# Performance work log

Measured on AMD Instinct MI355X. Metric: run time of the kernel, lower is better.

The kernel has to match this reference:

```python
import jax, jax.numpy as jnp
import numpy as np

KS = 5          # kernel_size per pseudo-dim
DIM = 2         # pseudo-coordinate dims
KTOT = KS ** DIM  # 25 spline kernel slots
N_NODES = 50000
N_EDGES = 1600000
N_GRAPHS = 64
F_IN, H1, H2, N_CLS = 32, 32, 64, 10


def spline_basis(edge_attr):
    """Open B-spline basis, degree 1, dim=2, kernel_size=5.
    Returns basis [E,4] and flat kernel indices [E,4]."""
    v = edge_attr * (KS - 1)                    # [E,2] in [0, KS-1]
    lo = jnp.floor(v)
    frac = v - lo                               # [E,2]
    lo_i = lo.astype(jnp.int32)
    # per-dim basis values for offsets s in {0,1}: (1-frac), frac
    bas_d = jnp.stack([1.0 - frac, frac], axis=-1)            # [E,2,2]
    idx_d = jnp.minimum(lo_i[..., None] + jnp.arange(2, dtype=jnp.int32), KS - 1)  # [E,2,2]
    basis = bas_d[:, 0, :, None] * bas_d[:, 1, None, :]       # [E,2,2]
    kidx = idx_d[:, 0, :, None] + KS * idx_d[:, 1, None, :]   # [E,2,2]
    E = edge_attr.shape[0]
    return basis.reshape(E, 4), kidx.reshape(E, 4)


def spline_conv(x, src, dst, basis, kidx, W, Wroot, b):
    """SplineConv: gather x[src], spline-weight, scatter-mean to dst, + root + bias.
    W: [KTOT, Cin, Cout]."""
    N, Cin = x.shape
    x_j = x[src]                                # [E, Cin] gather
    # accumulate per-(node, kernel-slot) weighted sums; loop over 4 nonzero combos
    T = jnp.zeros((N * KTOT, Cin), dtype=x.dtype)
    for s in range(4):
        seg = dst * KTOT + kidx[:, s]
        T = T + jax.ops.segment_sum(basis[:, s, None] * x_j, seg,
                                    num_segments=N * KTOT)
    T = T.reshape(N, KTOT, Cin)
    out = jnp.einsum('nki,kio->no', T, W)       # [N, Cout]
    deg = jax.ops.segment_sum(jnp.ones_like(dst, dtype=x.dtype), dst,
                              num_segments=N)
    out = out / jnp.maximum(deg, 1.0)[:, None]  # aggr='mean'
    return out + x @ Wroot + b


def global_mean_pool(x, batch, num_graphs):
    s = jax.ops.segment_sum(x, batch, num_segments=num_graphs)
    cnt = jax.ops.segment_sum(jnp.ones((x.shape[0],), x.dtype), batch,
                              num_segments=num_graphs)
    return s / jnp.maximum(cnt, 1.0)[:, None]


def setup_inputs() -> dict:
    key = jax.random.key(0)
    ks = jax.random.split(key, 16)
    x = jax.random.normal(ks[0], (N_NODES, F_IN), jnp.float32)
    edge_index = jax.random.randint(ks[1], (2, N_EDGES), 0, N_NODES, jnp.int32)
    edge_attr = jax.random.uniform(ks[2], (N_EDGES, DIM), jnp.float32)
    batch = jnp.sort(jax.random.randint(ks[3], (N_NODES,), 0, N_GRAPHS, jnp.int32))

    def w(k, shape, fan_in):
        return jax.random.normal(k, shape, jnp.float32) / np.sqrt(fan_in)

    return {
        'x': x, 'edge_index': edge_index, 'edge_attr': edge_attr, 'batch': batch,
        'W1': w(ks[4], (KTOT, F_IN, H1), F_IN), 'root1': w(ks[5], (F_IN, H1), F_IN),
        'b1': jnp.zeros((H1,), jnp.float32),
        'W2': w(ks[6], (KTOT, H1, H2), H1), 'root2': w(ks[7], (H1, H2), H1),
        'b2': jnp.zeros((H2,), jnp.float32),
        'lin1_w': w(ks[8], (H2, 64), H2), 'lin1_b': jnp.zeros((64,), jnp.float32),
        'lin2_w': w(ks[9], (64, 64), 64), 'lin2_b': jnp.zeros((64,), jnp.float32),
        'lin3_w': w(ks[10], (64, N_CLS), 64), 'lin3_b': jnp.zeros((N_CLS,), jnp.float32),
    }


def reference(x, edge_index, edge_attr, batch, W1, root1, b1, W2, root2, b2,
              lin1_w, lin1_b, lin2_w, lin2_b, lin3_w, lin3_b):
    src, dst = edge_index[0], edge_index[1]
    basis, kidx = spline_basis(edge_attr)
    h = jax.nn.relu(spline_conv(x, src, dst, basis, kidx, W1, root1, b1))
    h = jax.nn.relu(spline_conv(h, src, dst, basis, kidx, W2, root2, b2))
    g = global_mean_pool(h, batch, N_GRAPHS)                # [B, 64]
    g = g * jax.nn.sigmoid(g @ lin1_w + lin1_b)
    g = g * jax.nn.sigmoid(g @ lin2_w + lin2_b)
    return jax.nn.log_softmax(g @ lin3_w + lin3_b, axis=1)  # [B, N_CLS]
```

## Files before the change

kernel.cpp:

```cpp
#include <hip/hip_runtime.h>
#include <hip/hip_bf16.h>
#include <hip/hip_fp16.h>
#include <cstdint>


typedef _Float16 half8 __attribute__((ext_vector_type(8)));
typedef float f32x4 __attribute__((ext_vector_type(4)));

__device__ __forceinline__ int h2_as_int(__half2 h) {
  int v; __builtin_memcpy(&v, &h, 4); return v;
}
__device__ __forceinline__ __half2 int_as_h2(int v) {
  __half2 h; __builtin_memcpy(&h, &v, 4); return h;
}

__device__ __forceinline__ int lowb(const int* __restrict__ a, int n, int v) {
  int lo = 0, hi = n;
  while (lo < hi) { int m = (lo + hi) >> 1; if (a[m] < v) lo = m + 1; else hi = m; }
  return lo;
}

__global__ void hist_kernel(const int* __restrict__ dst, int E, int* __restrict__ deg) {
  int e = blockIdx.x * 256 + threadIdx.x;
  if (e < E) atomicAdd(&deg[dst[e]], 1);
}

__global__ __launch_bounds__(1024) void scan_block_kernel(
    const int* __restrict__ deg, int n, int* __restrict__ offs, int* __restrict__ bsums) {
  __shared__ int wsum[16];
  int t = threadIdx.x;
  int gi = blockIdx.x * 1024 + t;
  int v = (gi < n) ? deg[gi] : 0;
  int lane = t & 63, w = t >> 6;
  int x = v;
  #pragma unroll
  for (int d = 1; d < 64; d <<= 1) { int y = __shfl_up(x, d, 64); if (lane >= d) x += y; }
  if (lane == 63) wsum[w] = x;
  __syncthreads();
  if (w == 0) {
    int s = (lane < 16) ? wsum[lane] : 0;
    #pragma unroll
    for (int d = 1; d < 16; d <<= 1) { int y = __shfl_up(s, d, 64); if (lane >= d) s += y; }
    if (lane < 16) wsum[lane] = s;
  }
  __syncthreads();
  int add = (w > 0) ? wsum[w - 1] : 0;
  x += add;
  if (gi < n) offs[gi + 1] = x;
  if (t == 1023) bsums[blockIdx.x] = x;
}

__global__ __launch_bounds__(64) void scan_bsums_kernel(
    const int* __restrict__ bsums, int nb, int* __restrict__ boff) {
  int l = threadIdx.x;
  int v = (l < nb) ? bsums[l] : 0;
  int x = v;
  #pragma unroll
  for (int d = 1; d < 64; d <<= 1) { int y = __shfl_up(x, d, 64); if (l >= d) x += y; }
  if (l < nb) boff[l] = x - v;
}

__global__ void scan_add_kernel(int* __restrict__ offs, const int* __restrict__ boff, int n) {
  int i = blockIdx.x * 256 + threadIdx.x;
  if (i < n) offs[i + 1] += boff[i >> 10];
  if (i == 0) offs[0] = 0;
}

__global__ void scatter_kernel(const int* __restrict__ src, const int* __restrict__ dst,
                               const float2* __restrict__ attr, int E,
                               const int* __restrict__ offs, int* __restrict__ cursor,
                               int4* __restrict__ emeta) {
  int e = blockIdx.x * 256 + threadIdx.x;
  if (e < E) {
    float2 a = attr[e];
    float v0 = a.x * 4.f, v1 = a.y * 4.f;
    int i00 = min((int)v0, 3);
    int i10 = min((int)v1, 3);
    float f0 = v0 - (float)i00;
    float f1 = v1 - (float)i10;
    float w00 = (1.f - f0) * (1.f - f1);
    float w10 = f0 * (1.f - f1);
    float w01 = (1.f - f0) * f1;
    float w11 = f0 * f1;
    int d = dst[e];
    int p = offs[d] + atomicAdd(&cursor[d], 1);
    emeta[p] = make_int4(src[e], (i10 * 5 + i00) | (i10 << 5),
                         h2_as_int(__floats2half2_rn(w00, w10)),
                         h2_as_int(__floats2half2_rn(w01, w11)));
  }
}

__global__ void x2h_kernel(const float* __restrict__ X, __half* __restrict__ Xh, int n) {
  int i = blockIdx.x * 256 + threadIdx.x;
  if (i < n) Xh[i] = __float2half(X[i]);
}

__global__ void w2h_kernel(const float* __restrict__ W, __half* __restrict__ Wh,
                           int ncolTot, int COUT) {
  int idx = blockIdx.x * 256 + threadIdx.x;
  if (idx < ncolTot * 32) {
    int col = idx >> 5, i = idx & 31;
    int kk = col / COUT, ch = col - kk * COUT;
    Wh[idx] = __float2half(W[(kk * 32 + i) * COUT + ch]);
  }
}

__global__ __launch_bounds__(256) void mfma_ygemm(
    const __half* __restrict__ Xh, const __half* __restrict__ Wh,
    __half* __restrict__ Y, int N, int ncol, int strideY) {
  __shared__ __half Ls[16 * 264];
  const int t = threadIdx.x;
  const int w = t >> 6, lane = t & 63;
  const int rowBase = blockIdx.x * 16;
  const int colBase = blockIdx.y * 256;
  const int kOff = (lane >> 4) * 8;
  int arow = min(rowBase + (lane & 15), N - 1);
  const half8 Af = *(const half8*)(Xh + (size_t)arow * 32 + kOff);
  half8 Bf[4];
  #pragma unroll
  for (int c = 0; c < 4; ++c) {
    int col = min(colBase + w * 64 + c * 16 + (lane & 15), ncol - 1);
    Bf[c] = *(const half8*)(Wh + (size_t)col * 32 + kOff);
  }
  f32x4 zero = {0.f, 0.f, 0.f, 0.f};
  f32x4 acc[4];
  #pragma unroll
  for (int c = 0; c < 4; ++c)
    acc[c] = __builtin_amdgcn_mfma_f32_16x16x32_f16(Af, Bf[c], zero, 0, 0, 0);
  #pragma unroll
  for (int c = 0; c < 4; ++c) {
    int col = w * 64 + c * 16 + (lane & 15);
    int r0 = (lane >> 4) * 4;
    #pragma unroll
    for (int r = 0; r < 4; ++r)
      Ls[(r0 + r) * 264 + col] = __float2half(acc[c][r]);
  }
  __syncthreads();
  int row = rowBase + (t >> 4);
  int cseg = (t & 15) * 16;
  if (row < N && colBase + cseg < ncol) {
    int4* dst = (int4*)(Y + (size_t)row * (size_t)strideY + colBase + cseg);
    const int4* srcp = (const int4*)(Ls + (t >> 4) * 264 + cseg);
    dst[0] = srcp[0];
    dst[1] = srcp[1];
  }
}

template <int COUT>
__global__ __launch_bounds__(256) void gather_kernel(
    const int4* __restrict__ emeta, const int* __restrict__ offs,
    const __half* __restrict__ Y, int strideY,
    float* __restrict__ hagg, int N, int g0, int g1, int first, int fused,
    const __half* __restrict__ X, const float* __restrict__ root,
    const float* __restrict__ bias, __half* __restrict__ hout) {
  __shared__ float Rs[32 * COUT];
  const int t = threadIdx.x;
  if (fused) {
    #pragma unroll
    for (int q = 0; q < (8 * COUT) / 256; ++q)
      *(float4*)&Rs[(t + q * 256) * 4] = *(const float4*)&root[(t + q * 256) * 4];
    __syncthreads();
  }
  const int w = t >> 6, lane = t & 63;
  const int n = blockIdx.x * 4 + w;
  if (n >= N) return;
  const int q4 = lane >> 4, r = lane & 15;
  const int di0 = q4 & 1, di1 = q4 >> 1;
  constexpr int CPL = COUT / 16;
  const int laneByte = (di1 * 5 * COUT + di0 * COUT + r * CPL) * 2;
  const char* Ybase = (const char*)Y;
  float acc[CPL];
  #pragma unroll
  for (int j = 0; j < CPL; ++j) acc[j] = 0.f;
  const int beg = offs[n], end = offs[n + 1];
  for (int b0 = beg; b0 < end; b0 += 64) {
    const int cnt = min(64, end - b0);
    int4 m = emeta[b0 + min(lane, cnt - 1)];
    const int i10 = m.y >> 5;
    const bool valid = (lane < cnt) & (i10 >= g0) & (i10 < g1);
    int myByte = (m.x * strideY + ((m.y & 31) - g0 * 5) * COUT) * 2;
    int myP0 = m.z, myP1 = m.w;
    unsigned long long mask = __ballot(valid);
    while (mask) {
      int j = (int)__builtin_ctzll(mask);
      mask &= mask - 1;
      int b  = __builtin_amdgcn_readlane(myByte, j);
      int p0 = __builtin_amdgcn_readlane(myP0, j);
      int p1 = __builtin_amdgcn_readlane(myP1, j);
      __half2 wp = int_as_h2(di1 ? p1 : p0);
      float wq = __half2float(di0 ? __high2half(wp) : __low2half(wp));
      const __half* yp = (const __half*)(Ybase + (size_t)(unsigned)(b + laneByte));
      if constexpr (CPL == 2) {
        __half2 yv = *(const __half2*)yp;
        acc[0] = fmaf(wq, __half2float(__low2half(yv)), acc[0]);
        acc[1] = fmaf(wq, __half2float(__high2half(yv)), acc[1]);
      } else {
        __half2 ya = *(const __half2*)yp;
        __half2 yb = *(const __half2*)(yp + 2);
        acc[0] = fmaf(wq, __half2float(__low2half(ya)), acc[0]);
        acc[1] = fmaf(wq, __half2float(__high2half(ya)), acc[1]);
        acc[2] = fmaf(wq, __half2float(__low2half(yb)), acc[2]);
        acc[3] = fmaf(wq, __half2float(__high2half(yb)), acc[3]);
      }
    }
  }
  #pragma unroll
  for (int j = 0; j < CPL; ++j) {
    acc[j] += __shfl_xor(acc[j], 16);
    acc[j] += __shfl_xor(acc[j], 32);
  }
  const int laneCh = r * CPL;
  if (lane < 16) {
    if (!fused) {
      float* hp = hagg + (size_t)n * COUT + laneCh;
      if constexpr (CPL == 2) {
        float2 o = make_float2(acc[0], acc[1]);
        if (!first) { float2 p = *(float2*)hp; o.x += p.x; o.y += p.y; }
        *(float2*)hp = o;
      } else {
        float4 o = make_float4(acc[0], acc[1], acc[2], acc[3]);
        if (!first) {
          float4 p = *(float4*)hp;
          o.x += p.x; o.y += p.y; o.z += p.z; o.w += p.w;
        }
        *(float4*)hp = o;
      }
    } else {
      float rd = 1.f / (float)max(end - beg, 1);
      float a[CPL];
      #pragma unroll
      for (int j = 0; j < CPL; ++j) a[j] = acc[j] * rd;
      const __half* xr = X + (size_t)n * 32;
      for (int i = 0; i < 32; ++i) {
        float xv = __half2float(xr[i]);
        #pragma unroll
        for (int j = 0; j < CPL; ++j)
          a[j] = fmaf(xv, Rs[i * COUT + laneCh + j], a[j]);
      }
      #pragma unroll
      for (int j = 0; j < CPL; ++j) a[j] = fmaxf(a[j] + bias[laneCh + j], 0.f);
      __half2* op = (__half2*)(hout + (size_t)n * COUT + laneCh);
      #pragma unroll
      for (int p = 0; p < CPL / 2; ++p)
        op[p] = __floats2half2_rn(a[2 * p], a[2 * p + 1]);
    }
  }
}

template <int COUT>
__global__ __launch_bounds__(256) void finalize_kernel(
    const float* __restrict__ hagg, const __half* __restrict__ X,
    const float* __restrict__ root, const float* __restrict__ bias,
    const int* __restrict__ deg, __half* __restrict__ hout, int N) {
  __shared__ float Rs[32 * COUT];
  int t = threadIdx.x;
  #pragma unroll
  for (int q = 0; q < (32 * COUT) / 1024; ++q)
    *(float4*)&Rs[(q * 256 + t) * 4] = *(const float4*)&root[(q * 256 + t) * 4];
  __syncthreads();
  constexpr int TPN = COUT / 4;
  int gid = blockIdx.x * 256 + t;
  int n = gid / TPN;
  int c0 = (gid % TPN) * 4;
  if (n >= N) return;
  const __half* xr = X + (size_t)n * 32;
  float rd = 1.f / (float)max(deg[n], 1);
  float4 hv = *(const float4*)&hagg[(size_t)n * COUT + c0];
  float a0 = hv.x * rd, a1 = hv.y * rd, a2 = hv.z * rd, a3 = hv.w * rd;
  #pragma unroll
  for (int i = 0; i < 32; ++i) {
    float xv = __half2float(xr[i]);
    const float* rr = &Rs[i * COUT + c0];
    a0 = fmaf(xv, rr[0], a0);
    a1 = fmaf(xv, rr[1], a1);
    a2 = fmaf(xv, rr[2], a2);
    a3 = fmaf(xv, rr[3], a3);
  }
  __half2* op = (__half2*)(hout + (size_t)n * COUT + c0);
  op[0] = __floats2half2_rn(fmaxf(a0 + bias[c0 + 0], 0.f),
                            fmaxf(a1 + bias[c0 + 1], 0.f));
  op[1] = __floats2half2_rn(fmaxf(a2 + bias[c0 + 2], 0.f),
                            fmaxf(a3 + bias[c0 + 3], 0.f));
}

__global__ __launch_bounds__(256) void pool_kernel(
    const __half* __restrict__ h2, const int* __restrict__ batch, int N,
    float* __restrict__ poolacc) {
  __shared__ float red[4][64];
  int g = blockIdx.x >> 2, part = blockIdx.x & 3;
  int lo = lowb(batch, N, g), hi = lowb(batch, N, g + 1);
  int len = hi - lo;
  int b0 = lo + (int)(((long long)len * part) / 4);
  int b1 = lo + (int)(((long long)len * (part + 1)) / 4);
  int r = threadIdx.x >> 6, o = threadIdx.x & 63;
  float s = 0.f;
  for (int row = b0 + r; row < b1; row += 4)
    s += __half2float(h2[(size_t)row * 64 + o]);
  red[r][o] = s;
  __syncthreads();
  if (r == 0) {
    float v = red[0][o] + red[1][o] + red[2][o] + red[3][o];
    atomicAdd(&poolacc[g * 64 + o], v);
  }
}

__global__ __launch_bounds__(64) void head_kernel(
    const float* __restrict__ poolacc, const int* __restrict__ batch, int N,
    const float* __restrict__ w1, const float* __restrict__ b1,
    const float* __restrict__ w2, const float* __restrict__ b2,
    const float* __restrict__ w3, const float* __restrict__ b3,
    float* __restrict__ out) {
  __shared__ float gb[64];
  __shared__ float lg[10];
  int g = blockIdx.x, o = threadIdx.x;
  int lo = lowb(batch, N, g), hi = lowb(batch, N, g + 1);
  float cnt = fmaxf((float)(hi - lo), 1.f);
  float gv = poolacc[g * 64 + o] / cnt;
  gb[o] = gv;
  __syncthreads();
  float tacc = b1[o];
  for (int i = 0; i < 64; ++i) tacc = fmaf(gb[i], w1[i * 64 + o], tacc);
  gv = gv * (1.f / (1.f + expf(-tacc)));
  __syncthreads(); gb[o] = gv; __syncthreads();
  tacc = b2[o];
  for (int i = 0; i < 64; ++i) tacc = fmaf(gb[i], w2[i * 64 + o], tacc);
  gv = gv * (1.f / (1.f + expf(-tacc)));
  __syncthreads(); gb[o] = gv; __syncthreads();
  if (o < 10) {
    float l = b3[o];
    for (int i = 0; i < 64; ++i) l = fmaf(gb[i], w3[i * 10 + o], l);
    lg[o] = l;
  }
  __syncthreads();
  if (o < 10) {
    float m = lg[0];
    #pragma unroll
    for (int c = 1; c < 10; ++c) m = fmaxf(m, lg[c]);
    float s = 0.f;
    #pragma unroll
    for (int c = 0; c < 10; ++c) s += expf(lg[c] - m);
    out[g * 10 + o] = lg[o] - m - logf(s);
  }
}

extern "C" void kernel_launch(void* const* d_in, const int* in_sizes, int n_in,
                              void* d_out, int out_size, void* d_ws, size_t ws_size,
                              hipStream_t stream) {
  const float* x     = (const float*)d_in[0];
  const int*   ei    = (const int*)d_in[1];
  const float* eattr = (const float*)d_in[2];
  const int*   batch = (const int*)d_in[3];
  const float* W1    = (const float*)d_in[4];
  const float* root1 = (const float*)d_in[5];
  const float* b1    = (const float*)d_in[6];
  const float* W2    = (const float*)d_in[7];
  const float* root2 = (const float*)d_in[8];
  const float* b2    = (const float*)d_in[9];
  const float* l1w   = (const float*)d_in[10];
  const float* l1b   = (const float*)d_in[11];
  const float* l2w   = (const float*)d_in[12];
  const float* l2b   = (const float*)d_in[13];
  const float* l3w   = (const float*)d_in[14];
  const float* l3b   = (const float*)d_in[15];
  float* out = (float*)d_out;

  const int N = in_sizes[0] / 32;
  const int E = in_sizes[1] / 2;
  const int Npad = (N + 63) & ~63;

  char* base = (char*)d_ws;
  size_t off = 0;
  auto walloc = [&](size_t bytes) -> void* {
    off = (off + 255) & ~(size_t)255;
    void* p = base + off;
    off += bytes;
    return p;
  };
  int*    deg     = (int*)walloc((size_t)Npad * 4);
  int*    offs    = (int*)walloc((size_t)(N + 1) * 4);
  int*    cursor  = (int*)walloc((size_t)N * 4);
  int*    bsums   = (int*)walloc(64 * 4);
  int*    boff    = (int*)walloc(64 * 4);
  float*  poolacc = (float*)walloc(64 * 64 * 4);
  __half* h1h     = (__half*)walloc((size_t)N * 32 * 2);
  __half* h2h     = (__half*)walloc((size_t)N * 64 * 2);
  __half* Xh      = (__half*)walloc((size_t)N * 32 * 2);
  __half* Wh1     = (__half*)walloc((size_t)800 * 32 * 2);
  __half* Wh2     = (__half*)walloc((size_t)1600 * 32 * 2);
  float*  hagg    = (float*)walloc((size_t)N * 64 * 4);
  int4*   emeta   = (int4*)walloc((size_t)E * 16);
  off = (off + 255) & ~(size_t)255;
  size_t avail = (ws_size > off) ? (ws_size - off) : 0;
  __half* Yb = (__half*)(base + off);

  auto pickG = [&](int cout) -> int {
    size_t g5 = (size_t)N * 5 * cout * 2;
    if (avail < 2 * g5) return 0;
    size_t G = avail / g5 - 1;
    return (int)(G > 4 ? 4 : G);
  };
  int G1 = pickG(32), G2 = pickG(64);
  if (!G1 || !G2) return;

  const int* srcA = ei;
  const int* dstA = ei + E;

  hipMemsetAsync(deg, 0, (size_t)Npad * 4, stream);
  hipMemsetAsync(cursor, 0, (size_t)N * 4, stream);
  hipMemsetAsync(poolacc, 0, 64 * 64 * 4, stream);

  hist_kernel<<<(E + 255) / 256, 256, 0, stream>>>(dstA, E, deg);
  int nb = (N + 1023) / 1024;
  scan_block_kernel<<<nb, 1024, 0, stream>>>(deg, N, offs, bsums);
  scan_bsums_kernel<<<1, 64, 0, stream>>>(bsums, nb, boff);
  scan_add_kernel<<<(N + 255) / 256, 256, 0, stream>>>(offs, boff, N);
  scatter_kernel<<<(E + 255) / 256, 256, 0, stream>>>(srcA, dstA, (const float2*)eattr,
                                                      E, offs, cursor, emeta);
  x2h_kernel<<<((size_t)N * 32 + 255) / 256, 256, 0, stream>>>(x, Xh, N * 32);
  w2h_kernel<<<(800 * 32 + 255) / 256, 256, 0, stream>>>(W1, Wh1, 800, 32);
  w2h_kernel<<<(1600 * 32 + 255) / 256, 256, 0, stream>>>(W2, Wh2, 1600, 64);

  const int rowTiles = (N + 15) / 16;
  const int ggrid = (N + 3) / 4;
  for (int layer = 0; layer < 2; ++layer) {
    const __half* XinH = layer ? h1h : Xh;
    const __half* WhL  = layer ? Wh2 : Wh1;
    const float* rl    = layer ? root2 : root1;
    const float* bl    = layer ? b2 : b1;
    __half* HoutH      = layer ? h2h : h1h;
    const int G        = layer ? G2 : G1;
    const int COUT     = layer ? 64 : 32;
    const int fused    = (G >= 4) ? 1 : 0;
    for (int g0 = 0; g0 < 4; g0 += G) {
      int g1 = min(4, g0 + G);
      int kFirst = g0 * 5, kCount = (g1 - g0 + 1) * 5;
      int ncol = kCount * COUT;
      int first = (g0 == 0) ? 1 : 0;
      dim3 yg(rowTiles, (ncol + 255) / 256);
      mfma_ygemm<<<yg, 256, 0, stream>>>(XinH, WhL + (size_t)(kFirst * COUT) * 32,
                                         Yb, N, ncol, ncol);
      if (layer == 0)
        gather_kernel<32><<<ggrid, 256, 0, stream>>>(
            emeta, offs, Yb, ncol, hagg, N, g0, g1, first, fused,
            XinH, rl, bl, HoutH);
      else
        gather_kernel<64><<<ggrid, 256, 0, stream>>>(
            emeta, offs, Yb, ncol, hagg, N, g0, g1, first, fused,
            XinH, rl, bl, HoutH);
    }
    if (!fused) {
      if (layer == 0)
        finalize_kernel<32><<<((size_t)N * 8 + 255) / 256, 256, 0, stream>>>(
            hagg, XinH, rl, bl, deg, HoutH, N);
      else
        finalize_kernel<64><<<((size_t)N * 16 + 255) / 256, 256, 0, stream>>>(
            hagg, XinH, rl, bl, deg, HoutH, N);
    }
  }
  pool_kernel<<<256, 256, 0, stream>>>(h2h, batch, N, poolacc);
  head_kernel<<<64, 64, 0, stream>>>(poolacc, batch, N,
                                     l1w, l1b, l2w, l2b, l3w, l3b, out);
}
```

Baseline: 521.7 us.

## Store layer-2 spline GEMM output in FP8 and gather all 25 slots at once

The layer-2 precomputed Y = X·W table is now written as FP8 (1600 bytes per node), so both layers fit in one workspace pass without splitting kernel-slot groups. The gather loop drops ballot-based group filtering and processes edges in unrolled batches of four loads. The hagg/finalize fallback path is removed. This halves the bytes read by the layer-2 random gather and removes the multi-pass fallback, but FP8 rounding of Y lowers accuracy.

```diff
diff --git a/kernel.cpp b/kernel.cpp
--- a/kernel.cpp
+++ b/kernel.cpp
@@ -6,6 +6,7 @@
 
 typedef _Float16 half8 __attribute__((ext_vector_type(8)));
 typedef float f32x4 __attribute__((ext_vector_type(4)));
+typedef float f32x2 __attribute__((ext_vector_type(2)));
 
 __device__ __forceinline__ int h2_as_int(__half2 h) {
   int v; __builtin_memcpy(&v, &h, 4); return v;
@@ -84,7 +85,7 @@
     float w11 = f0 * f1;
     int d = dst[e];
     int p = offs[d] + atomicAdd(&cursor[d], 1);
-    emeta[p] = make_int4(src[e], (i10 * 5 + i00) | (i10 << 5),
+    emeta[p] = make_int4(src[e], i10 * 5 + i00,
                          h2_as_int(__floats2half2_rn(w00, w10)),
                          h2_as_int(__floats2half2_rn(w01, w11)));
   }
@@ -105,10 +106,13 @@
   }
 }
 
+template <bool FP8>
 __global__ __launch_bounds__(256) void mfma_ygemm(
     const __half* __restrict__ Xh, const __half* __restrict__ Wh,
-    __half* __restrict__ Y, int N, int ncol, int strideY) {
-  __shared__ __half Ls[16 * 264];
+    char* __restrict__ Y, int N, int ncol, int rowBytes) {
+  constexpr int EB = FP8 ? 1 : 2;
+  constexpr int LSTR = FP8 ? 272 : 528;
+  __shared__ __align__(16) char Ls[16 * LSTR];
   const int t = threadIdx.x;
   const int w = t >> 6, lane = t & 63;
   const int rowBase = blockIdx.x * 16;
@@ -132,43 +136,51 @@
     int col = w * 64 + c * 16 + (lane & 15);
     int r0 = (lane >> 4) * 4;
     #pragma unroll
-    for (int r = 0; r < 4; ++r)
-      Ls[(r0 + r) * 264 + col] = __float2half(acc[c][r]);
+    for (int r = 0; r < 4; ++r) {
+      if constexpr (FP8) {
+        int pk = __builtin_amdgcn_cvt_pk_fp8_f32(acc[c][r], acc[c][r], 0, false);
+        Ls[(r0 + r) * LSTR + col] = (char)(pk & 0xff);
+      } else {
+        *(__half*)(Ls + (r0 + r) * LSTR + col * 2) = __float2half(acc[c][r]);
+      }
+    }
   }
   __syncthreads();
   int row = rowBase + (t >> 4);
   int cseg = (t & 15) * 16;
   if (row < N && colBase + cseg < ncol) {
-    int4* dst = (int4*)(Y + (size_t)row * (size_t)strideY + colBase + cseg);
-    const int4* srcp = (const int4*)(Ls + (t >> 4) * 264 + cseg);
-    dst[0] = srcp[0];
-    dst[1] = srcp[1];
-  }
-}
-
-template <int COUT>
+    char* dst = Y + (size_t)row * rowBytes + (size_t)(colBase + cseg) * EB;
+    const char* s = Ls + (t >> 4) * LSTR + cseg * EB;
+    if constexpr (FP8) {
+      *(int4*)dst = *(const int4*)s;
+    } else {
+      ((int4*)dst)[0] = ((const int4*)s)[0];
+      ((int4*)dst)[1] = ((const int4*)s)[1];
+    }
+  }
+}
+
+template <int COUT, bool FP8>
 __global__ __launch_bounds__(256) void gather_kernel(
     const int4* __restrict__ emeta, const int* __restrict__ offs,
-    const __half* __restrict__ Y, int strideY,
-    float* __restrict__ hagg, int N, int g0, int g1, int first, int fused,
+    const char* __restrict__ Ybase, int rowBytes,
     const __half* __restrict__ X, const float* __restrict__ root,
-    const float* __restrict__ bias, __half* __restrict__ hout) {
+    const float* __restrict__ bias, __half* __restrict__ hout, int N) {
   __shared__ float Rs[32 * COUT];
   const int t = threadIdx.x;
-  if (fused) {
-    #pragma unroll
-    for (int q = 0; q < (8 * COUT) / 256; ++q)
-      *(float4*)&Rs[(t + q * 256) * 4] = *(const float4*)&root[(t + q * 256) * 4];
-    __syncthreads();
-  }
+  #pragma unroll
+  for (int q = 0; q < (8 * COUT) / 256; ++q)
+    *(float4*)&Rs[(t + q * 256) * 4] = *(const float4*)&root[(t + q * 256) * 4];
+  __syncthreads();
   const int w = t >> 6, lane = t & 63;
   const int n = blockIdx.x * 4 + w;
   if (n >= N) return;
   const int q4 = lane >> 4, r = lane & 15;
   const int di0 = q4 & 1, di1 = q4 >> 1;
   constexpr int CPL = COUT / 16;
-  const int laneByte = (di1 * 5 * COUT + di0 * COUT + r * CPL) * 2;
-  const char* Ybase = (const char*)Y;
+  constexpr int EB = FP8 ? 1 : 2;
+  const int laneByte = (di1 * 5 * COUT + di0 * COUT + r * CPL) * EB;
+  const int shiftSel = di0 * 16;
   float acc[CPL];
   #pragma unroll
   for (int j = 0; j < CPL; ++j) acc[j] = 0.f;
@@ -176,31 +188,38 @@
   for (int b0 = beg; b0 < end; b0 += 64) {
     const int cnt = min(64, end - b0);
     int4 m = emeta[b0 + min(lane, cnt - 1)];
-    const int i10 = m.y >> 5;
-    const bool valid = (lane < cnt) & (i10 >= g0) & (i10 < g1);
-    int myByte = (m.x * strideY + ((m.y & 31) - g0 * 5) * COUT) * 2;
-    int myP0 = m.z, myP1 = m.w;
-    unsigned long long mask = __ballot(valid);
-    while (mask) {
-      int j = (int)__builtin_ctzll(mask);
-      mask &= mask - 1;
-      int b  = __builtin_amdgcn_readlane(myByte, j);
-      int p0 = __builtin_amdgcn_readlane(myP0, j);
-      int p1 = __builtin_amdgcn_readlane(myP1, j);
-      __half2 wp = int_as_h2(di1 ? p1 : p0);
-      float wq = __half2float(di0 ? __high2half(wp) : __low2half(wp));
-      const __half* yp = (const __half*)(Ybase + (size_t)(unsigned)(b + laneByte));
-      if constexpr (CPL == 2) {
-        __half2 yv = *(const __half2*)yp;
-        acc[0] = fmaf(wq, __half2float(__low2half(yv)), acc[0]);
-        acc[1] = fmaf(wq, __half2float(__high2half(yv)), acc[1]);
-      } else {
-        __half2 ya = *(const __half2*)yp;
-        __half2 yb = *(const __half2*)(yp + 2);
-        acc[0] = fmaf(wq, __half2float(__low2half(ya)), acc[0]);
-        acc[1] = fmaf(wq, __half2float(__high2half(ya)), acc[1]);
-        acc[2] = fmaf(wq, __half2float(__low2half(yb)), acc[2]);
-        acc[3] = fmaf(wq, __half2float(__high2half(yb)), acc[3]);
+    const int myByte = m.x * rowBytes + m.y * (COUT * EB);
+    const int myP0 = m.z, myP1 = m.w;
+    for (int j0 = 0; j0 < cnt; j0 += 4) {
+      int yw[4]; float wq[4];
+      #pragma unroll
+      for (int u = 0; u < 4; ++u) {
+        int j = j0 + u;
+        int jc = (j < cnt) ? j : 0;
+        int b  = __builtin_amdgcn_readlane(myByte, jc);
+        int p0 = __builtin_amdgcn_readlane(myP0, jc);
+        int p1 = __builtin_amdgcn_readlane(myP1, jc);
+        int pw = (di1 ? p1 : p0) >> shiftSel;
+        unsigned short u16 = (unsigned short)pw;
+        __half hw; __builtin_memcpy(&hw, &u16, 2);
+        float wv = __half2float(hw);
+        wq[u] = (j < cnt) ? wv : 0.f;
+        yw[u] = *(const int*)(Ybase + (size_t)(unsigned)(b + laneByte));
+      }
+      #pragma unroll
+      for (int u = 0; u < 4; ++u) {
+        if constexpr (FP8) {
+          f32x2 fa = __builtin_amdgcn_cvt_pk_f32_fp8(yw[u], false);
+          f32x2 fb = __builtin_amdgcn_cvt_pk_f32_fp8(yw[u], true);
+          acc[0] = fmaf(wq[u], fa[0], acc[0]);
+          acc[1] = fmaf(wq[u], fa[1], acc[1]);
+          acc[2] = fmaf(wq[u], fb[0], acc[2]);
+          acc[3] = fmaf(wq[u], fb[1], acc[3]);
+        } else {
+          __half2 yv = int_as_h2(yw[u]);
+          acc[0] = fmaf(wq[u], __half2float(__low2half(yv)), acc[0]);
+          acc[1] = fmaf(wq[u], __half2float(__high2half(yv)), acc[1]);
+        }
       }
     }
   }
@@ -211,76 +230,24 @@
   }
   const int laneCh = r * CPL;
   if (lane < 16) {
-    if (!fused) {
-      float* hp = hagg + (size_t)n * COUT + laneCh;
-      if constexpr (CPL == 2) {
-        float2 o = make_float2(acc[0], acc[1]);
-        if (!first) { float2 p = *(float2*)hp; o.x += p.x; o.y += p.y; }
-        *(float2*)hp = o;
-      } else {
-        float4 o = make_float4(acc[0], acc[1], acc[2], acc[3]);
-        if (!first) {
-          float4 p = *(float4*)hp;
-          o.x += p.x; o.y += p.y; o.z += p.z; o.w += p.w;
-        }
-        *(float4*)hp = o;
-      }
-    } else {
-      float rd = 1.f / (float)max(end - beg, 1);
-      float a[CPL];
+    float rd = 1.f / (float)max(end - beg, 1);
+    float a[CPL];
+    #pragma unroll
+    for (int j = 0; j < CPL; ++j) a[j] = acc[j] * rd;
+    const __half* xr = X + (size_t)n * 32;
+    for (int i = 0; i < 32; ++i) {
+      float xv = __half2float(xr[i]);
       #pragma unroll
-      for (int j = 0; j < CPL; ++j) a[j] = acc[j] * rd;
-      const __half* xr = X + (size_t)n * 32;
-      for (int i = 0; i < 32; ++i) {
-        float xv = __half2float(xr[i]);
-        #pragma unroll
-        for (int j = 0; j < CPL; ++j)
-          a[j] = fmaf(xv, Rs[i * COUT + laneCh + j], a[j]);
-      }
-      #pragma unroll
-      for (int j = 0; j < CPL; ++j) a[j] = fmaxf(a[j] + bias[laneCh + j], 0.f);
-      __half2* op = (__half2*)(hout + (size_t)n * COUT + laneCh);
-      #pragma unroll
-      for (int p = 0; p < CPL / 2; ++p)
-        op[p] = __floats2half2_rn(a[2 * p], a[2 * p + 1]);
+      for (int j = 0; j < CPL; ++j)
+        a[j] = fmaf(xv, Rs[i * COUT + laneCh + j], a[j]);
     }
-  }
-}
-
-template <int COUT>
-__global__ __launch_bounds__(256) void finalize_kernel(
-    const float* __restrict__ hagg, const __half* __restrict__ X,
-    const float* __restrict__ root, const float* __restrict__ bias,
-    const int* __restrict__ deg, __half* __restrict__ hout, int N) {
-  __shared__ float Rs[32 * COUT];
-  int t = threadIdx.x;
-  #pragma unroll
-  for (int q = 0; q < (32 * COUT) / 1024; ++q)
-    *(float4*)&Rs[(q * 256 + t) * 4] = *(const float4*)&root[(q * 256 + t) * 4];
-  __syncthreads();
-  constexpr int TPN = COUT / 4;
-  int gid = blockIdx.x * 256 + t;
-  int n = gid / TPN;
-  int c0 = (gid % TPN) * 4;
-  if (n >= N) return;
-  const __half* xr = X + (size_t)n * 32;
-  float rd = 1.f / (float)max(deg[n], 1);
-  float4 hv = *(const float4*)&hagg[(size_t)n * COUT + c0];
-  float a0 = hv.x * rd, a1 = hv.y * rd, a2 = hv.z * rd, a3 = hv.w * rd;
-  #pragma unroll
-  for (int i = 0; i < 32; ++i) {
-    float xv = __half2float(xr[i]);
-    const float* rr = &Rs[i * COUT + c0];
-    a0 = fmaf(xv, rr[0], a0);
-    a1 = fmaf(xv, rr[1], a1);
-    a2 = fmaf(xv, rr[2], a2);
-    a3 = fmaf(xv, rr[3], a3);
-  }
-  __half2* op = (__half2*)(hout + (size_t)n * COUT + c0);
-  op[0] = __floats2half2_rn(fmaxf(a0 + bias[c0 + 0], 0.f),
-                            fmaxf(a1 + bias[c0 + 1], 0.f));
-  op[1] = __floats2half2_rn(fmaxf(a2 + bias[c0 + 2], 0.f),
-                            fmaxf(a3 + bias[c0 + 3], 0.f));
+    #pragma unroll
+    for (int j = 0; j < CPL; ++j) a[j] = fmaxf(a[j] + bias[laneCh + j], 0.f);
+    __half2* op = (__half2*)(hout + (size_t)n * COUT + laneCh);
+    #pragma unroll
+    for (int p = 0; p < CPL / 2; ++p)
+      op[p] = __floats2half2_rn(a[2 * p], a[2 * p + 1]);
+  }
 }
 
 __global__ __launch_bounds__(256) void pool_kernel(
@@ -387,20 +354,11 @@
   __half* Xh      = (__half*)walloc((size_t)N * 32 * 2);
   __half* Wh1     = (__half*)walloc((size_t)800 * 32 * 2);
   __half* Wh2     = (__half*)walloc((size_t)1600 * 32 * 2);
-  float*  hagg    = (float*)walloc((size_t)N * 64 * 4);
   int4*   emeta   = (int4*)walloc((size_t)E * 16);
   off = (off + 255) & ~(size_t)255;
   size_t avail = (ws_size > off) ? (ws_size - off) : 0;
-  __half* Yb = (__half*)(base + off);
-
-  auto pickG = [&](int cout) -> int {
-    size_t g5 = (size_t)N * 5 * cout * 2;
-    if (avail < 2 * g5) return 0;
-    size_t G = avail / g5 - 1;
-    return (int)(G > 4 ? 4 : G);
-  };
-  int G1 = pickG(32), G2 = pickG(64);
-  if (!G1 || !G2) return;
+  if (avail < (size_t)N * 1600) return;
+  char* Yb = base + off;
 
   const int* srcA = ei;
   const int* dstA = ei + E;
@@ -422,41 +380,17 @@
 
   const int rowTiles = (N + 15) / 16;
   const int ggrid = (N + 3) / 4;
-  for (int layer = 0; layer < 2; ++layer) {
-    const __half* XinH = layer ? h1h : Xh;
-    const __half* WhL  = layer ? Wh2 : Wh1;
-    const float* rl    = layer ? root2 : root1;
-    const float* bl    = layer ? b2 : b1;
-    __half* HoutH      = layer ? h2h : h1h;
-    const int G        = layer ? G2 : G1;
-    const int COUT     = layer ? 64 : 32;
-    const int fused    = (G >= 4) ? 1 : 0;
-    for (int g0 = 0; g0 < 4; g0 += G) {
-      int g1 = min(4, g0 + G);
-      int kFirst = g0 * 5, kCount = (g1 - g0 + 1) * 5;
-      int ncol = kCount * COUT;
-      int first = (g0 == 0) ? 1 : 0;
-      dim3 yg(rowTiles, (ncol + 255) / 256);
-      mfma_ygemm<<<yg, 256, 0, stream>>>(XinH, WhL + (size_t)(kFirst * COUT) * 32,
-                                         Yb, N, ncol, ncol);
-      if (layer == 0)
-        gather_kernel<32><<<ggrid, 256, 0, stream>>>(
-            emeta, offs, Yb, ncol, hagg, N, g0, g1, first, fused,
-            XinH, rl, bl, HoutH);
-      else
-        gather_kernel<64><<<ggrid, 256, 0, stream>>>(
-            emeta, offs, Yb, ncol, hagg, N, g0, g1, first, fused,
-            XinH, rl, bl, HoutH);
-    }
-    if (!fused) {
-      if (layer == 0)
-        finalize_kernel<32><<<((size_t)N * 8 + 255) / 256, 256, 0, stream>>>(
-            hagg, XinH, rl, bl, deg, HoutH, N);
-      else
-        finalize_kernel<64><<<((size_t)N * 16 + 255) / 256, 256, 0, stream>>>(
-            hagg, XinH, rl, bl, deg, HoutH, N);
-    }
-  }
+
+  mfma_ygemm<false><<<dim3(rowTiles, (800 + 255) / 256), 256, 0, stream>>>(
+      Xh, Wh1, Yb, N, 800, 1600);
+  gather_kernel<32, false><<<ggrid, 256, 0, stream>>>(
+      emeta, offs, Yb, 1600, Xh, root1, b1, h1h, N);
+
+  mfma_ygemm<true><<<dim3(rowTiles, (1600 + 255) / 256), 256, 0, stream>>>(
+      h1h, Wh2, Yb, N, 1600, 1600);
+  gather_kernel<64, true><<<ggrid, 256, 0, stream>>>(
+      emeta, offs, Yb, 1600, h1h, root2, b2, h2h, N);
+
   pool_kernel<<<256, 256, 0, stream>>>(h2h, batch, N, poolacc);
   head_kernel<<<64, 64, 0, stream>>>(poolacc, batch, N,
                                      l1w, l1b, l2w, l2b, l3w, l3b, out);
```

Measured after the change: 460.4 us. 11.8% less time.
